# Optimization experiments

Hardware: AMD Instinct MI355X
Metric: run time of the kernel (lower is better)

## Reference

```python
import jax, jax.numpy as jnp
import numpy as np

B, CIN, COUT, RES_IN, RES, LDIM = 16, 512, 512, 32, 64, 512
SQ2 = float(np.sqrt(2.0))   # relu def_gain
SQH = float(np.sqrt(0.5))   # residual gain
DN = ('NCHW', 'OIHW', 'NCHW')


def _f2d():
    # setup_filter([1,3,3,1]): normalize to sum 1, separable -> outer product
    f = jnp.array([1.0, 3.0, 3.0, 1.0], jnp.float32)
    f = f / f.sum()
    return jnp.outer(f, f)  # [4,4]


def _upfirdn(x, f2d, up, pad):
    # upfirdn2d: zero-upsample by `up` (zeros appended after each sample),
    # pad (pad0,pad1) per side, correlate with depthwise 4-tap filter.
    # lhs_dilation yields (H-1)*up+1, so fold the trailing up-1 zeros into right pad.
    C = x.shape[1]
    k = jnp.broadcast_to(f2d[None, None], (C, 1, 4, 4))
    p = (pad[0], pad[1] + up - 1)
    return jax.lax.conv_general_dilated(
        x, k, (1, 1), [p, p], lhs_dilation=(up, up),
        dimension_numbers=DN, feature_group_count=C)


def _affine(lat, w, b):
    # FullyConnectedLayer: weight_gain = 1/sqrt(in_features), bias_init handled in setup
    return lat @ (w * (1.0 / np.sqrt(w.shape[1]))).T + b


def _mod_demod(x, w, style):
    # modulate input, compute demod coefs: rsqrt(sum_i,k,k (w[o,i]*s[b,i])^2 + 1e-8)
    xm = x * style[:, :, None, None]
    d = jax.lax.rsqrt(
        jnp.einsum('bi,oi->bo', style * style, jnp.sum(w * w, axis=(2, 3))) + 1e-8)
    return xm, d


def setup_inputs():
    key = jax.random.key(0)
    ks = jax.random.split(key, 12)
    n = lambda k, s: jax.random.normal(k, s, jnp.float32)
    return dict(
        x=n(ks[0], (B, CIN, RES_IN, RES_IN)),
        latent1=n(ks[1], (B, 1, LDIM)),
        latent2=n(ks[2], (B, 2, LDIM)),
        aff0_w=n(ks[3], (CIN, LDIM)), aff0_b=jnp.ones((CIN,), jnp.float32),
        w0=n(ks[4], (COUT, CIN, 3, 3)), b0=jnp.zeros((COUT,), jnp.float32),
        nc0=n(ks[5], (RES, RES)), ns0=0.1 * n(ks[6], ()),
        aff1_w=n(ks[7], (COUT, LDIM)), aff1_b=jnp.ones((COUT,), jnp.float32),
        w1=n(ks[8], (COUT, COUT, 3, 3)), b1=jnp.zeros((COUT,), jnp.float32),
        nc1=n(ks[9], (RES, RES)), ns1=0.1 * n(ks[10], ()),
        skip_w=n(ks[11], (COUT, CIN, 1, 1)),
    )


def reference(x, latent1, latent2, aff0_w, aff0_b, w0, b0, nc0, ns0,
              aff1_w, aff1_b, w1, b1, nc1, ns1, skip_w):
    f2d = _f2d()
    # --- skip branch: Conv2dLayer(k=1, up=2, bias=False), gain sqrt(0.5) ---
    # conv2d_resample fast path: upfirdn(up=2, pad=(2,1), gain=up^2) then 1x1 conv
    xs = _upfirdn(x, f2d * 4.0, up=2, pad=(2, 1))              # [B,CIN,64,64]
    ws = skip_w * (1.0 / np.sqrt(CIN))                          # weight_gain, k=1
    y = jax.lax.conv_general_dilated(xs, ws, (1, 1), [(0, 0), (0, 0)],
                                     dimension_numbers=DN) * SQH
    # --- conv0: SynthesisLayer up=2 (modulated transposed conv + FIR) ---
    s0 = _affine(latent2[:, 0], aff0_w, aff0_b)                 # [B,CIN]
    h, d0 = _mod_demod(x, w0, s0)
    # torch conv_transpose2d(x, w0.T(0,1), stride=2, pad=0) == dilated conv,
    # pad k-1=2, kernel spatially flipped (flip_weight=False path)
    h = jax.lax.conv_general_dilated(h, jnp.flip(w0, (2, 3)), (1, 1),
                                     [(2, 2), (2, 2)], lhs_dilation=(2, 2),
                                     dimension_numbers=DN)      # [B,COUT,65,65]
    h = _upfirdn(h, f2d * 4.0, up=1, pad=(1, 1))                # [B,COUT,64,64]
    h = h * d0[:, :, None, None] + nc0 * ns0                    # demod + noise (fma)
    h = jax.nn.relu(h + b0[None, :, None, None]) * SQ2          # bias_act
    # --- conv1: SynthesisLayer up=1, gain sqrt(0.5) ---
    s1 = _affine(latent2[:, 1], aff1_w, aff1_b)                 # [B,COUT]
    h, d1 = _mod_demod(h, w1, s1)
    h = jax.lax.conv_general_dilated(h, w1, (1, 1), [(1, 1), (1, 1)],
                                     dimension_numbers=DN)
    h = h * d1[:, :, None, None] + nc1 * ns1
    h = jax.nn.relu(h + b1[None, :, None, None]) * (SQ2 * SQH)
    return y + h
```

## Files before the change

### kernel.cpp

```cpp
#include <hip/hip_runtime.h>
#include <hip/hip_bf16.h>


typedef __attribute__((ext_vector_type(8))) short short8;
typedef __attribute__((ext_vector_type(4))) float floatx4;

__device__ __forceinline__ float bf2f(__hip_bfloat16 v){ return __bfloat162float(v); }
__device__ __forceinline__ __hip_bfloat16 f2bf(float v){ return __float2bfloat16(v); }

__device__ __forceinline__ void glds16(const __hip_bfloat16* g, const short* l){
  __builtin_amdgcn_global_load_lds(
      (const __attribute__((address_space(1))) void*)g,
      (__attribute__((address_space(3))) void*)l,
      16, 0, 0);
}

__device__ __forceinline__ float ldin(const void* p, size_t i, int f32){
  return f32 ? ((const float*)p)[i] : bf2f(((const __hip_bfloat16*)p)[i]);
}

__global__ void k_detect(const void* __restrict__ x, int* __restrict__ flag){
  __shared__ int cnt;
  if (threadIdx.x == 0) cnt = 0;
  __syncthreads();
  const __hip_bfloat16* xb = (const __hip_bfloat16*)x;
  int c = 0;
  for (int i = threadIdx.x; i < 4096; i += 256){
    float v = bf2f(xb[i]);
    if (!(fabsf(v) < 1e6f)) c++;
  }
  atomicAdd(&cnt, c);
  __syncthreads();
  if (threadIdx.x == 0) *flag = (cnt > 8) ? 1 : 0;
}

__global__ void k_misc(const void* __restrict__ nc0, const void* __restrict__ nc1,
                       const void* __restrict__ b0,  const void* __restrict__ b1,
                       const void* __restrict__ ns0, const void* __restrict__ ns1,
                       const int* __restrict__ flag,
                       float* __restrict__ nf0, float* __restrict__ nf1,
                       float* __restrict__ b0f, float* __restrict__ b1f,
                       float* __restrict__ scf, float* __restrict__ zbuf){
  const int f32 = *flag;
  int i = blockIdx.x*256 + threadIdx.x;
  if (i < 4096)       nf0[i]      = ldin(nc0, i, f32);
  else if (i < 8192)  nf1[i-4096] = ldin(nc1, i-4096, f32);
  else if (i < 8704)  b0f[i-8192] = ldin(b0, i-8192, f32);
  else if (i < 9216)  b1f[i-8704] = ldin(b1, i-8704, f32);
  else if (i == 9216) scf[0]      = ldin(ns0, 0, f32);
  else if (i == 9217) scf[1]      = ldin(ns1, 0, f32);
  else if (i >= 9232 && i < 9744) zbuf[i-9232] = 0.0f;
}


__global__ void k_wsum(const void* __restrict__ w0, const void* __restrict__ w1,
                       const int* __restrict__ flag,
                       float* __restrict__ wsum0, float* __restrict__ wsum1){
  const int f32 = *flag;
  int idx = blockIdx.x*256 + threadIdx.x;
  float a = 0.f, b = 0.f;
  #pragma unroll
  for(int t=0;t<9;t++){
    float v0 = ldin(w0, (size_t)idx*9+t, f32); a += v0*v0;
    float v1 = ldin(w1, (size_t)idx*9+t, f32); b += v1*v1;
  }
  wsum0[idx] = a; wsum1[idx] = b;
}

__global__ void k_styles(const void* __restrict__ lat2,
                         const void* __restrict__ aw0, const void* __restrict__ ab0,
                         const void* __restrict__ aw1, const void* __restrict__ ab1,
                         const int* __restrict__ flag,
                         float* __restrict__ s0, float* __restrict__ s1){
  const int f32 = *flag;
  int idx = blockIdx.x*256 + threadIdx.x;
  if (idx >= 16*512) return;
  int b = idx>>9, o = idx&511;
  float a0 = 0.f, a1 = 0.f;
  for(int i=0;i<512;i++){
    a0 += ldin(lat2, (size_t)b*1024 + i,       f32) * ldin(aw0, (size_t)o*512+i, f32);
    a1 += ldin(lat2, (size_t)b*1024 + 512 + i, f32) * ldin(aw1, (size_t)o*512+i, f32);
  }
  const float inv = 0.04419417382415922f;
  s0[idx] = a0*inv + ldin(ab0, o, f32);
  s1[idx] = a1*inv + ldin(ab1, o, f32);
}

__global__ void k_demod(const float* __restrict__ s0, const float* __restrict__ s1,
                        const float* __restrict__ wsum0, const float* __restrict__ wsum1,
                        float* __restrict__ d0, float* __restrict__ d1){
  int idx = blockIdx.x*256 + threadIdx.x;
  if (idx >= 16*512) return;
  int b = idx>>9, o = idx&511;
  float a0 = 0.f, a1 = 0.f;
  for(int i=0;i<512;i++){
    float t0 = s0[b*512+i]; a0 += t0*t0*wsum0[o*512+i];
    float t1 = s1[b*512+i]; a1 += t1*t1*wsum1[o*512+i];
  }
  d0[idx] = rsqrtf(a0 + 1e-8f);
  d1[idx] = rsqrtf(a1 + 1e-8f);
}

__global__ void k_xprep(const void* __restrict__ x, const int* __restrict__ flag,
                        __hip_bfloat16* __restrict__ xT){
  const int f32 = *flag;
  int tid = blockIdx.x*256 + threadIdx.x;
  int ci = tid&511; int r = tid>>9;
  int xx = r&31; r >>= 5; int yy = r&31; int b = r>>5;
  xT[tid] = f2bf(ldin(x, (size_t)(((b*512+ci)*32+yy)*32+xx), f32));
}

__global__ void k_xmod(__hip_bfloat16* __restrict__ xT,
                       const float* __restrict__ s0){
  int tid = blockIdx.x*256 + threadIdx.x;
  int ci = tid&511; int b = tid>>19;
  xT[tid] = f2bf(bf2f(xT[tid]) * s0[b*512+ci]);
}

__global__ void k_w0prep(const void* __restrict__ w0, const int* __restrict__ flag,
                         __hip_bfloat16* __restrict__ W0p){
  const int f32 = *flag;
  int idx = blockIdx.x*256 + threadIdx.x;
  int oc = idx>>9, ci = idx&511;
  const float g[4] = {0.25f, 0.75f, 0.75f, 0.25f};
  float K2[6][6] = {};
  #pragma unroll
  for(int ty=0;ty<3;ty++)
    #pragma unroll
    for(int tx=0;tx<3;tx++){
      float w = ldin(w0, (size_t)idx*9 + (2-ty)*3 + (2-tx), f32);
      #pragma unroll
      for(int qy=0;qy<4;qy++)
        #pragma unroll
        for(int qx=0;qx<4;qx++)
          K2[qy+ty][qx+tx] += g[qy]*g[qx]*w;
    }
  #pragma unroll
  for(int Py=0;Py<2;Py++)
    #pragma unroll
    for(int Px=0;Px<2;Px++){
      int cls = Py*2+Px;
      #pragma unroll
      for(int jy=0;jy<3;jy++)
        #pragma unroll
        for(int jx=0;jx<3;jx++){
          int sy = (1-Py) + 2*jy, sx = (1-Px) + 2*jx;
          W0p[((size_t)(cls*9 + jy*3+jx)*512 + oc)*512 + ci] = f2bf(K2[sy][sx]);
        }
    }
}

__global__ void k_w1prep(const void* __restrict__ w1, const void* __restrict__ skw,
                         const int* __restrict__ flag,
                         __hip_bfloat16* __restrict__ w1T,
                         __hip_bfloat16* __restrict__ wskipT){
  const int f32 = *flag;
  int idx = blockIdx.x*256 + threadIdx.x;
  int oc = idx>>9, ci = idx&511;
  #pragma unroll
  for(int t=0;t<9;t++)
    w1T[((size_t)t*512 + oc)*512 + ci] = f2bf(ldin(w1, (size_t)idx*9+t, f32));
  wskipT[idx] = f2bf(ldin(skw, idx, f32) * 0.03125f);
}

template<int TAPS, int MODE, int H>
__launch_bounds__(256,2)
__global__ void k_gemm(const __hip_bfloat16* __restrict__ Ain,
                       const __hip_bfloat16* __restrict__ Wt,
                       const float* __restrict__ dvec,
                       const float* __restrict__ noise,
                       const float* __restrict__ nscal,
                       const float* __restrict__ bias,
                       const float* __restrict__ s1,
                       const __hip_bfloat16* __restrict__ tlow,
                       const __hip_bfloat16* __restrict__ zbuf,
                       void* __restrict__ Outv){
  constexpr int LOGH = (H==32)?5:6;
  __shared__ short As[128*32];
  __shared__ short Bs[128*32];
  const int t = threadIdx.x;
  const int Mbase = blockIdx.x*128;
  const int Nbase = blockIdx.y*128;
  const int cls = blockIdx.z;
  const __hip_bfloat16* Wslab = Wt + (size_t)cls * TAPS * 512 * 512;

  const int wave = t>>6, lane = t&63;
  const int wm = (wave>>1)*64, wn = (wave&1)*64;
  const int lm = lane&15, lk = (lane>>4)*8;

  const int rsub = lane>>2;
  const int koff = (lane&3)*8;
  const int row0 = wave*16 + rsub;
  const int row1 = row0 + 64;
  short* ldsA0 = As + wave*512;
  short* ldsA1 = As + (wave+4)*512;
  short* ldsB0 = Bs + wave*512;
  short* ldsB1 = Bs + (wave+4)*512;

  floatx4 acc[4][4];
  #pragma unroll
  for(int i=0;i<4;i++)
    #pragma unroll
    for(int j=0;j<4;j++)
      #pragma unroll
      for(int r=0;r<4;r++) acc[i][j][r] = 0.0f;

  const int m0 = Mbase + row0, m1 = Mbase + row1;
  const int b0p = m0 >> (2*LOGH), b1p = m1 >> (2*LOGH);
  const int py0 = (m0 >> LOGH)&(H-1), py1 = (m1 >> LOGH)&(H-1);
  const int px0 = m0 & (H-1),        px1 = m1 & (H-1);

  #pragma unroll 1
  for(int tap=0; tap<TAPS; ++tap){
    const int dy = (TAPS==1)?0:(tap/3 - 1);
    const int dx = (TAPS==1)?0:(tap%3 - 1);
    const int iy0 = py0+dy, ix0 = px0+dx, iy1 = py1+dy, ix1 = px1+dx;
    const bool v0 = ((unsigned)iy0 < (unsigned)H) && ((unsigned)ix0 < (unsigned)H);
    const bool v1 = ((unsigned)iy1 < (unsigned)H) && ((unsigned)ix1 < (unsigned)H);
    const __hip_bfloat16* pA0 = v0 ? (Ain + ((((b0p*H + iy0)*H + ix0) << 9) + koff))
                                   : (zbuf + koff);
    const __hip_bfloat16* pA1 = v1 ? (Ain + ((((b1p*H + iy1)*H + ix1) << 9) + koff))
                                   : (zbuf + koff);
    const __hip_bfloat16* wt  = Wslab + (size_t)tap*512*512;
    const __hip_bfloat16* pB0 = wt + (Nbase + row0)*512 + koff;
    const __hip_bfloat16* pB1 = wt + (Nbase + row1)*512 + koff;

    #pragma unroll 1
    for(int kk=0; kk<512; kk+=32){
      glds16(pA0, ldsA0);
      glds16(pA1, ldsA1);
      glds16(pB0, ldsB0);
      glds16(pB1, ldsB1);
      __syncthreads();
      short8 af[4], bf[4];
      #pragma unroll
      for(int i=0;i<4;i++) af[i] = *(const short8*)&As[(wm + i*16 + lm)*32 + lk];
      #pragma unroll
      for(int j=0;j<4;j++) bf[j] = *(const short8*)&Bs[(wn + j*16 + lm)*32 + lk];
      #pragma unroll
      for(int i=0;i<4;i++)
        #pragma unroll
        for(int j=0;j<4;j++)
          acc[i][j] = __builtin_amdgcn_mfma_f32_16x16x32_bf16(af[i], bf[j], acc[i][j], 0,0,0);
      __syncthreads();
      pA0 += 32; pA1 += 32; pB0 += 32; pB1 += 32;
    }
  }

  const float nsv = (MODE>=1) ? nscal[0] : 0.0f;
  #pragma unroll
  for(int i=0;i<4;i++){
    #pragma unroll
    for(int j=0;j<4;j++){
      const int mt = Mbase + wm + i*16 + (lane>>4)*4;
      const int n  = Nbase + wn + j*16 + lm;
      #pragma unroll
      for(int r=0;r<4;r++){
        const int m = mt + r;
        float val = acc[i][j][r];
        if constexpr (MODE==0){
          ((__hip_bfloat16*)Outv)[(size_t)m*512 + n] = f2bf(val);
        } else if constexpr (MODE==1){
          const int b = m>>10, uy = (m>>5)&31, ux = m&31;
          const int py = 2*uy + (cls>>1), px = 2*ux + (cls&1);
          val = val*dvec[b*512+n] + noise[py*64+px]*nsv + bias[n];
          val = fmaxf(val, 0.0f) * 1.4142135623730951f * s1[b*512+n];
          ((__hip_bfloat16*)Outv)[(size_t)((b*64+py)*64+px)*512 + n] = f2bf(val);
        } else {
          const int b = m>>12, py = (m>>6)&63, px = m&63;
          val = val*dvec[b*512+n] + noise[py*64+px]*nsv + bias[n];
          val = fmaxf(val, 0.0f);
          const int uy = py>>1, ay = py&1, ux2 = px>>1, ax = px&1;
          const int ry = uy - 1 + ay, rx = ux2 - 1 + ax;
          const float cy0 = ay ? 0.75f : 0.25f, cy1 = ay ? 0.25f : 0.75f;
          const float cx0 = ax ? 0.75f : 0.25f, cx1 = ax ? 0.25f : 0.75f;
          float yv = 0.0f;
          #pragma unroll
          for(int e=0;e<2;e++){
            const int yy = ry + e;
            if ((unsigned)yy >= 32u) continue;
            const float cy = e ? cy1 : cy0;
            #pragma unroll
            for(int f=0;f<2;f++){
              const int xx = rx + f;
              if ((unsigned)xx >= 32u) continue;
              const float cx = f ? cx1 : cx0;
              yv += cy*cx*bf2f(tlow[(size_t)((b*32+yy)*32+xx)*512 + n]);
            }
          }
          val += yv;
          ((float*)Outv)[(size_t)((b*512 + n)*64 + py)*64 + px] = val;
        }
      }
    }
  }
}


extern "C" void kernel_launch(void* const* d_in, const int* in_sizes, int n_in,
                              void* d_out, int out_size, void* d_ws, size_t ws_size,
                              hipStream_t stream){
  (void)in_sizes; (void)n_in; (void)out_size; (void)ws_size;
  const void* x    = d_in[0];
  const void* lat2 = d_in[2];
  const void* aw0  = d_in[3];
  const void* ab0  = d_in[4];
  const void* w0   = d_in[5];
  const void* b0   = d_in[6];
  const void* nc0  = d_in[7];
  const void* ns0  = d_in[8];
  const void* aw1  = d_in[9];
  const void* ab1  = d_in[10];
  const void* w1   = d_in[11];
  const void* b1   = d_in[12];
  const void* nc1  = d_in[13];
  const void* ns1  = d_in[14];
  const void* skw  = d_in[15];

  char* p = (char*)d_ws;
  float* s0v   = (float*)p; p += 16*512*4;
  float* s1v   = (float*)p; p += 16*512*4;
  float* d0v   = (float*)p; p += 16*512*4;
  float* d1v   = (float*)p; p += 16*512*4;
  float* nf0   = (float*)p; p += 4096*4;
  float* nf1   = (float*)p; p += 4096*4;
  float* b0f   = (float*)p; p += 512*4;
  float* b1f   = (float*)p; p += 512*4;
  float* scf   = (float*)p; p += 16;
  int*   flag  = (int*)p;   p += 16;
  float* zbuf  = (float*)p; p += 512*4;
  __hip_bfloat16* w1T    = (__hip_bfloat16*)p; p += (size_t)9*512*512*2;
  __hip_bfloat16* wskipT = (__hip_bfloat16*)p; p += (size_t)512*512*2;
  __hip_bfloat16* tlow   = (__hip_bfloat16*)p; p += (size_t)16*32*32*512*2;
  __hip_bfloat16* xT     = (__hip_bfloat16*)p; p += (size_t)16*32*32*512*2;
  __hip_bfloat16* W0p    = (__hip_bfloat16*)p; p += (size_t)4*9*512*512*2;
  __hip_bfloat16* act0m  = (__hip_bfloat16*)p; p += (size_t)16*64*64*512*2;
  float* wsum0 = (float*)act0m;
  float* wsum1 = (float*)act0m + 512*512;

  const __hip_bfloat16* zb = (const __hip_bfloat16*)zbuf;

  k_detect<<<   1, 256, 0, stream>>>(x, flag);
  k_misc  <<<  39, 256, 0, stream>>>(nc0, nc1, b0, b1, ns0, ns1, flag,
                                     nf0, nf1, b0f, b1f, scf, zbuf);
  k_wsum  <<<1024, 256, 0, stream>>>(w0, w1, flag, wsum0, wsum1);
  k_styles<<<  32, 256, 0, stream>>>(lat2, aw0, ab0, aw1, ab1, flag, s0v, s1v);
  k_demod <<<  32, 256, 0, stream>>>(s0v, s1v, wsum0, wsum1, d0v, d1v);
  k_xprep <<<32768,256, 0, stream>>>(x, flag, xT);
  k_w0prep<<<1024, 256, 0, stream>>>(w0, flag, W0p);
  k_w1prep<<<1024, 256, 0, stream>>>(w1, skw, flag, w1T, wskipT);

  k_gemm<1,0,32><<<dim3(128,4,1), 256, 0, stream>>>(
      xT, wskipT, nullptr, nullptr, nullptr, nullptr, nullptr, nullptr, zb, tlow);
  k_xmod  <<<32768,256, 0, stream>>>(xT, s0v);
  k_gemm<9,1,32><<<dim3(128,4,4), 256, 0, stream>>>(
      xT, W0p, d0v, nf0, scf, b0f, s1v, nullptr, zb, act0m);
  k_gemm<9,2,64><<<dim3(512,4,1), 256, 0, stream>>>(
      act0m, w1T, d1v, nf1, scf+1, b1f, nullptr, tlow, zb, d_out);
}
```

Before: 1.678 ms.

## Double-buffer LDS tiles to overlap global loads with MFMA compute

The GEMM main loop now uses two LDS buffers for A and B. The next K-slice is issued with global_load_lds while the current slice is being computed, and the two nested tap/kk loops are flattened into a single loop with one barrier per iteration instead of two. The goal is to hide global memory latency behind the matrix instructions. In exchange, LDS use per block doubles to 32KB, which may reduce occupancy.

```diff
diff --git a/kernel.cpp b/kernel.cpp
--- a/kernel.cpp
+++ b/kernel.cpp
@@ -176,8 +176,8 @@
                        const __hip_bfloat16* __restrict__ zbuf,
                        void* __restrict__ Outv){
   constexpr int LOGH = (H==32)?5:6;
-  __shared__ short As[128*32];
-  __shared__ short Bs[128*32];
+  __shared__ short As[2][128*32];
+  __shared__ short Bs[2][128*32];
   const int t = threadIdx.x;
   const int Mbase = blockIdx.x*128;
   const int Nbase = blockIdx.y*128;
@@ -192,10 +192,6 @@
   const int koff = (lane&3)*8;
   const int row0 = wave*16 + rsub;
   const int row1 = row0 + 64;
-  short* ldsA0 = As + wave*512;
-  short* ldsA1 = As + (wave+4)*512;
-  short* ldsB0 = Bs + wave*512;
-  short* ldsB1 = Bs + (wave+4)*512;
 
   floatx4 acc[4][4];
   #pragma unroll
@@ -209,43 +205,53 @@
   const int b0p = m0 >> (2*LOGH), b1p = m1 >> (2*LOGH);
   const int py0 = (m0 >> LOGH)&(H-1), py1 = (m1 >> LOGH)&(H-1);
   const int px0 = m0 & (H-1),        px1 = m1 & (H-1);
-
-  #pragma unroll 1
-  for(int tap=0; tap<TAPS; ++tap){
+  const int gb0 = (Nbase + row0)*512 + koff;
+  const int gb1 = (Nbase + row1)*512 + koff;
+
+  auto STAGE = [&](int ks, int buf){
+    const int tap = (TAPS==1) ? 0 : (ks>>4);
+    const int kk  = (ks & 15) << 5;
     const int dy = (TAPS==1)?0:(tap/3 - 1);
     const int dx = (TAPS==1)?0:(tap%3 - 1);
     const int iy0 = py0+dy, ix0 = px0+dx, iy1 = py1+dy, ix1 = px1+dx;
     const bool v0 = ((unsigned)iy0 < (unsigned)H) && ((unsigned)ix0 < (unsigned)H);
     const bool v1 = ((unsigned)iy1 < (unsigned)H) && ((unsigned)ix1 < (unsigned)H);
-    const __hip_bfloat16* pA0 = v0 ? (Ain + ((((b0p*H + iy0)*H + ix0) << 9) + koff))
+    const __hip_bfloat16* pA0 = v0 ? (Ain + ((((b0p*H + iy0)*H + ix0) << 9) + kk + koff))
                                    : (zbuf + koff);
-    const __hip_bfloat16* pA1 = v1 ? (Ain + ((((b1p*H + iy1)*H + ix1) << 9) + koff))
+    const __hip_bfloat16* pA1 = v1 ? (Ain + ((((b1p*H + iy1)*H + ix1) << 9) + kk + koff))
                                    : (zbuf + koff);
-    const __hip_bfloat16* wt  = Wslab + (size_t)tap*512*512;
-    const __hip_bfloat16* pB0 = wt + (Nbase + row0)*512 + koff;
-    const __hip_bfloat16* pB1 = wt + (Nbase + row1)*512 + koff;
-
-    #pragma unroll 1
-    for(int kk=0; kk<512; kk+=32){
-      glds16(pA0, ldsA0);
-      glds16(pA1, ldsA1);
-      glds16(pB0, ldsB0);
-      glds16(pB1, ldsB1);
-      __syncthreads();
-      short8 af[4], bf[4];
-      #pragma unroll
-      for(int i=0;i<4;i++) af[i] = *(const short8*)&As[(wm + i*16 + lm)*32 + lk];
-      #pragma unroll
-      for(int j=0;j<4;j++) bf[j] = *(const short8*)&Bs[(wn + j*16 + lm)*32 + lk];
-      #pragma unroll
-      for(int i=0;i<4;i++)
-        #pragma unroll
-        for(int j=0;j<4;j++)
-          acc[i][j] = __builtin_amdgcn_mfma_f32_16x16x32_bf16(af[i], bf[j], acc[i][j], 0,0,0);
-      __syncthreads();
-      pA0 += 32; pA1 += 32; pB0 += 32; pB1 += 32;
-    }
-  }
+    const __hip_bfloat16* wt  = Wslab + (size_t)tap*262144 + kk;
+    glds16(pA0, As[buf] + wave*512);
+    glds16(pA1, As[buf] + (wave+4)*512);
+    glds16(wt + gb0, Bs[buf] + wave*512);
+    glds16(wt + gb1, Bs[buf] + (wave+4)*512);
+  };
+
+  auto COMPUTE = [&](int buf){
+    short8 af[4], bfr[4];
+    #pragma unroll
+    for(int i=0;i<4;i++) af[i]  = *(const short8*)&As[buf][(wm + i*16 + lm)*32 + lk];
+    #pragma unroll
+    for(int j=0;j<4;j++) bfr[j] = *(const short8*)&Bs[buf][(wn + j*16 + lm)*32 + lk];
+    #pragma unroll
+    for(int i=0;i<4;i++)
+      #pragma unroll
+      for(int j=0;j<4;j++)
+        acc[i][j] = __builtin_amdgcn_mfma_f32_16x16x32_bf16(af[i], bfr[j], acc[i][j], 0,0,0);
+  };
+
+  const int NKS = TAPS*16;
+  STAGE(0, 0);
+  __syncthreads();
+  int cur = 0;
+  #pragma unroll 1
+  for(int ks=0; ks<NKS-1; ++ks){
+    STAGE(ks+1, cur^1);
+    COMPUTE(cur);
+    __syncthreads();
+    cur ^= 1;
+  }
+  COMPUTE(cur);
 
   const float nsv = (MODE>=1) ? nscal[0] : 0.0f;
   #pragma unroll
```

After: 1.696 ms. Within noise of the previous version (+1.0%).
